# Kernel optimization log

Measured on AMD Instinct MI355X. Metric: run time of the kernel, lower is better.

## Reference

```python
import jax, jax.numpy as jnp
import numpy as np

N_NODES = 50000
N_EDGES = 500000
H = 128
N_LAYERS = 3


def _mlp_params(key, in_dim, h_dim, out_dim):
    k1, k2 = jax.random.split(key)
    s1 = 1.0 / np.sqrt(in_dim)
    s2 = 1.0 / np.sqrt(h_dim)
    return (jax.random.uniform(k1, (in_dim, h_dim), jnp.float32, -s1, s1),
            jnp.zeros((h_dim,), jnp.float32),
            jax.random.uniform(k2, (h_dim, out_dim), jnp.float32, -s2, s2),
            jnp.zeros((out_dim,), jnp.float32))


def setup_inputs() -> dict:
    key = jax.random.key(0)
    ks = jax.random.split(key, 8)
    x = jax.random.normal(ks[0], (N_NODES, H), jnp.float32)
    edge_attr = jax.random.normal(ks[1], (N_EDGES, H), jnp.float32)
    pos = jax.random.normal(ks[2], (N_NODES, 3), jnp.float32)
    src = jax.random.randint(ks[3], (N_EDGES,), 0, N_NODES)
    # avoid self-loops so rel_dist > 0 (original assumes no zero-length edges)
    off = jax.random.randint(ks[4], (N_EDGES,), 1, N_NODES)
    dst = (src + off) % N_NODES
    edge_index = jnp.stack([src, dst]).astype(jnp.int64)
    # per-layer MLP params, stacked over layers
    msg, acc, nod = [], [], []
    for i in range(N_LAYERS):
        kk = jax.random.fold_in(ks[5], i)
        ka, kb, kc = jax.random.split(kk, 3)
        msg.append(_mlp_params(ka, 3 * H, H, H))       # message_mlp
        acc.append(_mlp_params(kb, H, 2 * H, 1))       # accl_mlp
        nod.append(_mlp_params(kc, 2 * H, 2 * H, H))   # node_mlp
    stack = lambda ps: tuple(jnp.stack([p[j] for p in ps]) for j in range(4))
    mW1, mb1, mW2, mb2 = stack(msg)
    aW1, ab1, aW2, ab2 = stack(acc)
    nW1, nb1, nW2, nb2 = stack(nod)
    return dict(x=x, edge_index=edge_index, edge_attr=edge_attr, pos=pos,
                msg_W1=mW1, msg_b1=mb1, msg_W2=mW2, msg_b2=mb2,
                acc_W1=aW1, acc_b1=ab1, acc_W2=aW2, acc_b2=ab2,
                node_W1=nW1, node_b1=nb1, node_W2=nW2, node_b2=nb2)


def _mlp(h, W1, b1, W2, b2):
    return jax.nn.relu(h @ W1 + b1) @ W2 + b2


def reference(x, edge_index, edge_attr, pos,
              msg_W1, msg_b1, msg_W2, msg_b2,
              acc_W1, acc_b1, acc_W2, acc_b2,
              node_W1, node_b1, node_W2, node_b2):
    src, dst = edge_index[0], edge_index[1]
    n = x.shape[0]
    deg = jax.ops.segment_sum(jnp.ones((src.shape[0],), x.dtype), dst, num_segments=n)
    denom = jnp.maximum(deg, 1.0)[:, None]
    for l in range(N_LAYERS):
        # message: cat(x_i=dst, x_j=src, edge_attr) -> MLP
        m_in = jnp.concatenate([x[dst], x[src], edge_attr], axis=-1)  # [E, 3H]
        m = _mlp(m_in, msg_W1[l], msg_b1[l], msg_W2[l], msg_b2[l])    # [E, H]
        # equivariant acceleration update
        w = _mlp(m, acc_W1[l], acc_b1[l], acc_W2[l], acc_b2[l])       # [E, 1]
        rel = pos[src] - pos[dst]                                     # [E, 3]
        dist = jnp.sqrt(jnp.sum(rel * rel, axis=-1, keepdims=True))
        acc_e = w * rel / dist
        pos = pos + jax.ops.segment_sum(acc_e, dst, num_segments=n) / denom
        # node update (beta_x = 1.0 -> x_out = x_update)
        intra = jax.ops.segment_sum(m, dst, num_segments=n) / denom   # [N, H]
        x = _mlp(jnp.concatenate([x, intra], axis=-1),
                 node_W1[l], node_b1[l], node_W2[l], node_b2[l])
    return pos
```

## Files before the change

kernel.cpp:

```cpp
#include <hip/hip_runtime.h>
#include <hip/hip_bf16.h>
#include <math.h>

#define N_NODES 50000
#define N_EDGES 500000
#define H 128
#define NL 3
#define SCAN_B 256
#define NCHUNK ((N_NODES + SCAN_B - 1) / SCAN_B)

typedef short short8v __attribute__((ext_vector_type(8)));
typedef float f32x4 __attribute__((ext_vector_type(4)));
typedef unsigned short ushort8v __attribute__((ext_vector_type(8)));
typedef unsigned short ushort4v __attribute__((ext_vector_type(4)));

__device__ __forceinline__ unsigned short f2b(float f) {
  __hip_bfloat16 h = __float2bfloat16(f);
  return __builtin_bit_cast(unsigned short, h);
}
__device__ __forceinline__ float b2f(unsigned short s) {
  unsigned u = (unsigned)s << 16;
  return __builtin_bit_cast(float, u);
}


__global__ void k_deg_i(const int* __restrict__ dst, int* __restrict__ degC) {
  int e = blockIdx.x * blockDim.x + threadIdx.x;
  if (e < N_EDGES) atomicAdd(&degC[dst[e]], 1);
}

__global__ void k_inv(const int* __restrict__ degC, float* __restrict__ invd) {
  int i = blockIdx.x * blockDim.x + threadIdx.x;
  if (i < N_NODES) invd[i] = 1.0f / fmaxf((float)degC[i], 1.0f);
}

__global__ void k_scan1(const int* __restrict__ degC, int* __restrict__ cursor,
                        int* __restrict__ chunkSum) {
  __shared__ int s[SCAN_B];
  int t = threadIdx.x, i = blockIdx.x * SCAN_B + t;
  int v = (i < N_NODES) ? degC[i] : 0;
  s[t] = v;
  __syncthreads();
  for (int o = 1; o < SCAN_B; o <<= 1) {
    int u = (t >= o) ? s[t - o] : 0;
    __syncthreads();
    s[t] += u;
    __syncthreads();
  }
  if (i < N_NODES) cursor[i] = s[t] - v;
  if (t == SCAN_B - 1) chunkSum[blockIdx.x] = s[t];
}

__global__ void k_scan2(int* __restrict__ chunkSum) {
  __shared__ int s[SCAN_B];
  int t = threadIdx.x;
  int v = (t < NCHUNK) ? chunkSum[t] : 0;
  s[t] = v;
  __syncthreads();
  for (int o = 1; o < SCAN_B; o <<= 1) {
    int u = (t >= o) ? s[t - o] : 0;
    __syncthreads();
    s[t] += u;
    __syncthreads();
  }
  if (t < NCHUNK) chunkSum[t] = s[t] - v;
}

__global__ void k_scan3(int* __restrict__ cursor, const int* __restrict__ chunkSum) {
  int i = blockIdx.x * SCAN_B + threadIdx.x;
  if (i < N_NODES) cursor[i] += chunkSum[blockIdx.x];
}

__global__ void k_scatter_sort(const int* __restrict__ dst, int* __restrict__ cursor,
                               int* __restrict__ sorted) {
  int e = blockIdx.x * blockDim.x + threadIdx.x;
  if (e < N_EDGES) {
    int p = atomicAdd(&cursor[dst[e]], 1);
    sorted[p] = e;
  }
}


__global__ void k_cvt_x(const float* __restrict__ x, unsigned short* __restrict__ xb, int n4) {
  int i = blockIdx.x * blockDim.x + threadIdx.x;
  if (i < n4) {
    float4 v = ((const float4*)x)[i];
    ushort4v o;
    o[0] = f2b(v.x); o[1] = f2b(v.y); o[2] = f2b(v.z); o[3] = f2b(v.w);
    ((ushort4v*)xb)[i] = o;
  }
}

__global__ void k_cvt_wt(const float* __restrict__ src, unsigned short* __restrict__ dst,
                         int K, int N, int total) {
  int i = blockIdx.x * blockDim.x + threadIdx.x;
  if (i < total) {
    int l = i / (K * N);
    int rem = i - l * K * N;
    int k = rem / N;
    int n = rem - k * N;
    dst[((size_t)l * N + n) * K + k] = f2b(src[i]);
  }
}

#define MFMA_STEP(AP, APITCH, AKOFF, ACCN)                                         \
  { _Pragma("unroll")                                                              \
    for (int ks = 0; ks < 2; ++ks) {                                               \
      short8v af_ = *(const short8v*)&AP[(wv * 16 + ln15) * APITCH + (AKOFF) + ks * 32 + quad * 8]; \
      _Pragma("unroll")                                                            \
      for (int nt = 0; nt < 8; ++nt) {                                             \
        short8v bf_ = *(const short8v*)&sB[(nt * 16 + ln15) * 72 + ks * 32 + quad * 8]; \
        ACCN[nt] = __builtin_amdgcn_mfma_f32_16x16x32_bf16(af_, bf_, ACCN[nt], 0, 0, 0); \
      } } }

#define STAGE_B(EXPR)                                                              \
  { _Pragma("unroll")                                                              \
    for (int i_ = 0; i_ < 4; ++i_) {                                               \
      int flat_ = tid + i_ * 256;                                                  \
      int n = flat_ >> 3, seg = flat_ & 7;                                         \
      *(float4*)&sB[n * 72 + seg * 8] = *(const float4*)&(EXPR);                   \
    } }


__launch_bounds__(256, 3)
__global__ void k_edge(const unsigned short* __restrict__ xb,
                       const float* __restrict__ pos,
                       const float* __restrict__ eattr,
                       const int* __restrict__ srcI,
                       const int* __restrict__ dstI,
                       const int* __restrict__ sorted,
                       const unsigned short* __restrict__ mW1t, const float* __restrict__ mb1,
                       const unsigned short* __restrict__ mW2t, const float* __restrict__ mb2,
                       const unsigned short* __restrict__ aW1t, const float* __restrict__ ab1,
                       const float* __restrict__ aW2, const float* __restrict__ ab2,
                       float* __restrict__ intra,
                       float* __restrict__ pdelta,
                       int do_intra)
{
  __shared__ unsigned short sA[64 * 72];
  __shared__ unsigned short sB[128 * 72];
  __shared__ unsigned short sM[64 * 136];
  __shared__ int sEid[64], sSrc[64], sDst[64];
  __shared__ float sW[64];
  __shared__ float sPE[64 * 3];

  const int tid = threadIdx.x;
  const int e0 = blockIdx.x * 64;
  const int nv = min(N_EDGES - e0, 64);
  if (tid < 64) {
    int idx = min(e0 + tid, N_EDGES - 1);
    int eid = sorted[idx];
    sEid[tid] = eid; sSrc[tid] = srcI[eid]; sDst[tid] = dstI[eid];
  }
  __syncthreads();

  const int wv = tid >> 6, lane = tid & 63, quad = lane >> 4, ln15 = lane & 15;

  f32x4 acc[8];
#pragma unroll
  for (int nt = 0; nt < 8; ++nt) acc[nt] = (f32x4){0.f, 0.f, 0.f, 0.f};

  for (int c = 0; c < 6; ++c) {
#pragma unroll
    for (int i_ = 0; i_ < 2; ++i_) {
      int flat_ = tid + i_ * 256;
      int row = flat_ >> 3, seg = flat_ & 7;
      if (c < 4) {
        int node = (c < 2) ? sDst[row] : sSrc[row];
        const unsigned short* sp = xb + (size_t)node * H + (c & 1) * 64 + seg * 8;
        *(float4*)&sA[row * 72 + seg * 8] = *(const float4*)sp;
      } else {
        const float* ep = eattr + (size_t)sEid[row] * H + (c - 4) * 64 + seg * 8;
        float4 p0 = *(const float4*)ep;
        float4 p1 = *(const float4*)(ep + 4);
        ushort8v v;
        v[0] = f2b(p0.x); v[1] = f2b(p0.y); v[2] = f2b(p0.z); v[3] = f2b(p0.w);
        v[4] = f2b(p1.x); v[5] = f2b(p1.y); v[6] = f2b(p1.z); v[7] = f2b(p1.w);
        *(ushort8v*)&sA[row * 72 + seg * 8] = v;
      }
    }
    STAGE_B(mW1t[(size_t)n * 384 + c * 64 + seg * 8])
    __syncthreads();
    MFMA_STEP(sA, 72, 0, acc)
    __syncthreads();
  }

#pragma unroll
  for (int nt = 0; nt < 8; ++nt) {
    int col = nt * 16 + ln15;
    float bb = mb1[col];
#pragma unroll
    for (int r = 0; r < 4; ++r) {
      int row = wv * 16 + quad * 4 + r;
      sM[row * 136 + col] = f2b(fmaxf(acc[nt][r] + bb, 0.f));
      acc[nt][r] = 0.f;
    }
  }
  __syncthreads();

  for (int c = 0; c < 2; ++c) {
    STAGE_B(mW2t[(size_t)n * 128 + c * 64 + seg * 8])
    __syncthreads();
    MFMA_STEP(sM, 136, c * 64, acc)
    __syncthreads();
  }

#pragma unroll
  for (int nt = 0; nt < 8; ++nt) {
    int col = nt * 16 + ln15;
    float bb = mb2[col];
#pragma unroll
    for (int r = 0; r < 4; ++r) {
      int row = wv * 16 + quad * 4 + r;
      sM[row * 136 + col] = f2b(acc[nt][r] + bb);
    }
  }
  __syncthreads();

  float wp0 = 0.f, wp1 = 0.f, wp2 = 0.f, wp3 = 0.f;
  for (int h = 0; h < 2; ++h) {
#pragma unroll
    for (int nt = 0; nt < 8; ++nt) acc[nt] = (f32x4){0.f, 0.f, 0.f, 0.f};
    for (int c = 0; c < 2; ++c) {
      STAGE_B(aW1t[((size_t)h * 128 + n) * 128 + c * 64 + seg * 8])
      __syncthreads();
      MFMA_STEP(sM, 136, c * 64, acc)
      __syncthreads();
    }
#pragma unroll
    for (int nt = 0; nt < 8; ++nt) {
      int col = h * 128 + nt * 16 + ln15;
      float bb = ab1[col], a2 = aW2[col];
      wp0 += fmaxf(acc[nt][0] + bb, 0.f) * a2;
      wp1 += fmaxf(acc[nt][1] + bb, 0.f) * a2;
      wp2 += fmaxf(acc[nt][2] + bb, 0.f) * a2;
      wp3 += fmaxf(acc[nt][3] + bb, 0.f) * a2;
    }
  }
#pragma unroll
  for (int m = 1; m <= 8; m <<= 1) {
    wp0 += __shfl_xor(wp0, m, 64);
    wp1 += __shfl_xor(wp1, m, 64);
    wp2 += __shfl_xor(wp2, m, 64);
    wp3 += __shfl_xor(wp3, m, 64);
  }
  if (ln15 == 0) {
    float b2 = ab2[0];
    sW[wv * 16 + quad * 4 + 0] = wp0 + b2;
    sW[wv * 16 + quad * 4 + 1] = wp1 + b2;
    sW[wv * 16 + quad * 4 + 2] = wp2 + b2;
    sW[wv * 16 + quad * 4 + 3] = wp3 + b2;
  }
  __syncthreads();

  if (tid < nv) {
    int s = sSrc[tid], d = sDst[tid];
    float rx = pos[s * 3 + 0] - pos[d * 3 + 0];
    float ry = pos[s * 3 + 1] - pos[d * 3 + 1];
    float rz = pos[s * 3 + 2] - pos[d * 3 + 2];
    float dist = sqrtf(rx * rx + ry * ry + rz * rz);
    float cf = sW[tid] / dist;
    sPE[tid * 3 + 0] = cf * rx;
    sPE[tid * 3 + 1] = cf * ry;
    sPE[tid * 3 + 2] = cf * rz;
  }
  __syncthreads();

  if (tid < 3) {
    float run = 0.0f;
    int cur = -2;
    for (int e = 0; e < 64; ++e) {
      int d = (e < nv) ? sDst[e] : -1;
      if (d != cur) {
        if (cur >= 0 && run != 0.0f) atomicAdd(&pdelta[cur * 3 + tid], run);
        run = 0.0f;
        cur = d;
      }
      if (d >= 0) run += sPE[e * 3 + tid];
    }
    if (cur >= 0 && run != 0.0f) atomicAdd(&pdelta[cur * 3 + tid], run);
  }

  if (do_intra) {
    int f = tid & 127;
    int hf = tid >> 7;
    int eBeg = hf * 32, eEnd = eBeg + 32;
    float run = 0.0f;
    int cur = -2;
    for (int e = eBeg; e < eEnd; ++e) {
      int d = (e < nv) ? sDst[e] : -1;
      if (d != cur) {
        if (cur >= 0 && run != 0.0f) atomicAdd(&intra[(size_t)cur * H + f], run);
        run = 0.0f;
        cur = d;
      }
      if (d >= 0) run += b2f(sM[e * 136 + f]);
    }
    if (cur >= 0 && run != 0.0f) atomicAdd(&intra[(size_t)cur * H + f], run);
  }
}


__launch_bounds__(256, 3)
__global__ void k_node(const unsigned short* __restrict__ xb,
                       const float* __restrict__ intra,
                       const float* __restrict__ invd,
                       const unsigned short* __restrict__ nW1t, const float* __restrict__ nb1,
                       const unsigned short* __restrict__ nW2t, const float* __restrict__ nb2,
                       const float* __restrict__ pos_in,
                       const float* __restrict__ pdelta,
                       unsigned short* __restrict__ xb_out,
                       float* __restrict__ pos_out,
                       int compute_x)
{
  __shared__ unsigned short sA[64 * 72];
  __shared__ unsigned short sB[128 * 72];
  __shared__ unsigned short sH[64 * 136];
  const int tid = threadIdx.x;
  const int n0 = blockIdx.x * 64;

  if (tid < 192) {
    int n = n0 + tid / 3, cc = tid % 3;
    if (n < N_NODES)
      pos_out[n * 3 + cc] = pos_in[n * 3 + cc] + pdelta[n * 3 + cc] * invd[n];
  }
  if (!compute_x) return;

  const int wv = tid >> 6, lane = tid & 63, quad = lane >> 4, ln15 = lane & 15;

  f32x4 xacc[8];
#pragma unroll
  for (int nt = 0; nt < 8; ++nt) xacc[nt] = (f32x4){0.f, 0.f, 0.f, 0.f};

  f32x4 acc[8];
  for (int h = 0; h < 2; ++h) {
#pragma unroll
    for (int nt = 0; nt < 8; ++nt) acc[nt] = (f32x4){0.f, 0.f, 0.f, 0.f};
    for (int c = 0; c < 4; ++c) {
#pragma unroll
      for (int i_ = 0; i_ < 2; ++i_) {
        int flat_ = tid + i_ * 256;
        int row = flat_ >> 3, seg = flat_ & 7;
        int n = min(n0 + row, N_NODES - 1);
        if (c < 2) {
          *(float4*)&sA[row * 72 + seg * 8] =
              *(const float4*)&xb[(size_t)n * H + c * 64 + seg * 8];
        } else {
          const float* ip = intra + (size_t)n * H + (c - 2) * 64 + seg * 8;
          float iv = invd[n];
          float4 p0 = *(const float4*)ip;
          float4 p1 = *(const float4*)(ip + 4);
          ushort8v v;
          v[0] = f2b(p0.x * iv); v[1] = f2b(p0.y * iv);
          v[2] = f2b(p0.z * iv); v[3] = f2b(p0.w * iv);
          v[4] = f2b(p1.x * iv); v[5] = f2b(p1.y * iv);
          v[6] = f2b(p1.z * iv); v[7] = f2b(p1.w * iv);
          *(ushort8v*)&sA[row * 72 + seg * 8] = v;
        }
      }
      STAGE_B(nW1t[((size_t)h * 128 + n) * 256 + c * 64 + seg * 8])
      __syncthreads();
      MFMA_STEP(sA, 72, 0, acc)
      __syncthreads();
    }
#pragma unroll
    for (int nt = 0; nt < 8; ++nt) {
      int col = nt * 16 + ln15;
      float bb = nb1[h * 128 + col];
#pragma unroll
      for (int r = 0; r < 4; ++r) {
        int row = wv * 16 + quad * 4 + r;
        sH[row * 136 + col] = f2b(fmaxf(acc[nt][r] + bb, 0.f));
      }
    }
    __syncthreads();
    for (int c2 = 0; c2 < 2; ++c2) {
      STAGE_B(nW2t[(size_t)n * 256 + h * 128 + c2 * 64 + seg * 8])
      __syncthreads();
      MFMA_STEP(sH, 136, c2 * 64, xacc)
      __syncthreads();
    }
  }
#pragma unroll
  for (int nt = 0; nt < 8; ++nt) {
    int col = nt * 16 + ln15;
    float bb = nb2[col];
#pragma unroll
    for (int r = 0; r < 4; ++r) {
      int row = n0 + wv * 16 + quad * 4 + r;
      if (row < N_NODES)
        xb_out[(size_t)row * H + col] = f2b(xacc[nt][r] + bb);
    }
  }
}

extern "C" void kernel_launch(void* const* d_in, const int* in_sizes, int n_in,
                              void* d_out, int out_size, void* d_ws, size_t ws_size,
                              hipStream_t stream) {
  const float* x0    = (const float*)d_in[0];
  const int*   eidx  = (const int*)d_in[1];
  const float* eattr = (const float*)d_in[2];
  const float* pos0  = (const float*)d_in[3];
  const float* mW1 = (const float*)d_in[4];
  const float* mb1 = (const float*)d_in[5];
  const float* mW2 = (const float*)d_in[6];
  const float* mb2 = (const float*)d_in[7];
  const float* aW1 = (const float*)d_in[8];
  const float* ab1 = (const float*)d_in[9];
  const float* aW2 = (const float*)d_in[10];
  const float* ab2 = (const float*)d_in[11];
  const float* nW1 = (const float*)d_in[12];
  const float* nb1 = (const float*)d_in[13];
  const float* nW2 = (const float*)d_in[14];
  const float* nb2 = (const float*)d_in[15];
  const int* srcI = eidx;
  const int* dstI = eidx + N_EDGES;

  char* wsb = (char*)d_ws;
  int*   degC    = (int*)wsb;                     wsb += (size_t)N_NODES * 4;
  int*   cursor  = (int*)wsb;                     wsb += (size_t)N_NODES * 4;
  int*   chunkS  = (int*)wsb;                     wsb += 256 * 4;
  int*   sorted  = (int*)wsb;                     wsb += (size_t)N_EDGES * 4;
  float* invd    = (float*)wsb;                   wsb += (size_t)N_NODES * 4;
  float* pdelta  = (float*)wsb;                   wsb += (size_t)3 * N_NODES * 4;
  float* pos_a   = (float*)wsb;                   wsb += (size_t)3 * N_NODES * 4;
  float* pos_b   = (float*)wsb;                   wsb += (size_t)3 * N_NODES * 4;
  float* intra   = (float*)wsb;                   wsb += (size_t)N_NODES * H * 4;
  unsigned short* xb0  = (unsigned short*)wsb;    wsb += (size_t)N_NODES * H * 2;
  unsigned short* xb_a = (unsigned short*)wsb;    wsb += (size_t)N_NODES * H * 2;
  unsigned short* xb_b = (unsigned short*)wsb;    wsb += (size_t)N_NODES * H * 2;
  unsigned short* mW1t = (unsigned short*)wsb;    wsb += (size_t)NL * 128 * 384 * 2;
  unsigned short* mW2t = (unsigned short*)wsb;    wsb += (size_t)NL * 128 * 128 * 2;
  unsigned short* aW1t = (unsigned short*)wsb;    wsb += (size_t)NL * 256 * 128 * 2;
  unsigned short* nW1t = (unsigned short*)wsb;    wsb += (size_t)NL * 256 * 256 * 2;
  unsigned short* nW2t = (unsigned short*)wsb;    wsb += (size_t)NL * 128 * 256 * 2;

  hipMemsetAsync(degC, 0, N_NODES * sizeof(int), stream);
  k_deg_i<<<(N_EDGES + 255) / 256, 256, 0, stream>>>(dstI, degC);
  k_inv<<<(N_NODES + 255) / 256, 256, 0, stream>>>(degC, invd);
  k_scan1<<<NCHUNK, SCAN_B, 0, stream>>>(degC, cursor, chunkS);
  k_scan2<<<1, SCAN_B, 0, stream>>>(chunkS);
  k_scan3<<<NCHUNK, SCAN_B, 0, stream>>>(cursor, chunkS);
  k_scatter_sort<<<(N_EDGES + 255) / 256, 256, 0, stream>>>(dstI, cursor, sorted);

  {
    int n4 = N_NODES * H / 4;
    k_cvt_x<<<(n4 + 255) / 256, 256, 0, stream>>>(x0, xb0, n4);
    int t1 = NL * 384 * 128;
    k_cvt_wt<<<(t1 + 255) / 256, 256, 0, stream>>>(mW1, mW1t, 384, 128, t1);
    int t2 = NL * 128 * 128;
    k_cvt_wt<<<(t2 + 255) / 256, 256, 0, stream>>>(mW2, mW2t, 128, 128, t2);
    int t3 = NL * 128 * 256;
    k_cvt_wt<<<(t3 + 255) / 256, 256, 0, stream>>>(aW1, aW1t, 128, 256, t3);
    int t4 = NL * 256 * 256;
    k_cvt_wt<<<(t4 + 255) / 256, 256, 0, stream>>>(nW1, nW1t, 256, 256, t4);
    int t5 = NL * 256 * 128;
    k_cvt_wt<<<(t5 + 255) / 256, 256, 0, stream>>>(nW2, nW2t, 256, 128, t5);
  }

  const unsigned short* xc = xb0;
  const float* pc = pos0;
  float* pos_out_final = (float*)d_out;

  for (int l = 0; l < NL; ++l) {
    int last = (l == NL - 1);
    hipMemsetAsync(pdelta, 0, 3 * N_NODES * sizeof(float), stream);
    if (!last)
      hipMemsetAsync(intra, 0, (size_t)N_NODES * H * sizeof(float), stream);

    k_edge<<<(N_EDGES + 63) / 64, 256, 0, stream>>>(
        xc, pc, eattr, srcI, dstI, sorted,
        mW1t + (size_t)l * 128 * 384, mb1 + (size_t)l * 128,
        mW2t + (size_t)l * 128 * 128, mb2 + (size_t)l * 128,
        aW1t + (size_t)l * 256 * 128, ab1 + (size_t)l * 256,
        aW2 + (size_t)l * 256, ab2 + l,
        intra, pdelta, last ? 0 : 1);

    float* pn = last ? pos_out_final : (l == 0 ? pos_a : pos_b);
    unsigned short* xn = (l == 0) ? xb_a : xb_b;
    k_node<<<(N_NODES + 63) / 64, 256, 0, stream>>>(
        xc, intra, invd,
        nW1t + (size_t)l * 256 * 256, nb1 + (size_t)l * 256,
        nW2t + (size_t)l * 128 * 256, nb2 + (size_t)l * 128,
        pc, pdelta, xn, pn, last ? 0 : 1);

    xc = xn;
    pc = pn;
  }
}
```

Before: 1.386 ms.

## Precompute per-node projections of the message MLP's first layer

The first message-MLP layer is split by linearity. The x_dst and x_src parts are computed once per node in a new k_xab kernel and stored as bf16. Each edge then gathers and adds the two projected rows and only runs the edge_attr part of the GEMM (K=128 instead of 384). This cuts per-edge MFMA work and replaces gathers of raw features with gathers of precomputed projections. The costs are an extra kernel, a 256-wide bf16 buffer, and extra bf16 rounding of the partial sums. It also loads edge_attr A fragments directly into registers and raises the launch-bounds occupancy hint from 3 to 4.

```diff
diff --git a/kernel.cpp b/kernel.cpp
--- a/kernel.cpp
+++ b/kernel.cpp
@@ -122,8 +122,57 @@
     } }
 
 
-__launch_bounds__(256, 3)
-__global__ void k_edge(const unsigned short* __restrict__ xb,
+__launch_bounds__(256, 4)
+__global__ void k_xab(const unsigned short* __restrict__ xb,
+                      const unsigned short* __restrict__ mW1t,
+                      unsigned short* __restrict__ xab)
+{
+  __shared__ unsigned short sB[128 * 72];
+  const int tid = threadIdx.x;
+  const int n0 = blockIdx.x * 64;
+  const int wv = tid >> 6, lane = tid & 63, quad = lane >> 4, ln15 = lane & 15;
+  const int arow = min(n0 + wv * 16 + ln15, N_NODES - 1);
+
+  short8v afr[2][2];
+#pragma unroll
+  for (int c = 0; c < 2; ++c)
+#pragma unroll
+    for (int ks = 0; ks < 2; ++ks)
+      afr[c][ks] = *(const short8v*)&xb[(size_t)arow * H + c * 64 + ks * 32 + quad * 8];
+
+  for (int h = 0; h < 2; ++h) {
+    f32x4 acc[8];
+#pragma unroll
+    for (int nt = 0; nt < 8; ++nt) acc[nt] = (f32x4){0.f, 0.f, 0.f, 0.f};
+    for (int c = 0; c < 2; ++c) {
+      STAGE_B(mW1t[(size_t)n * 384 + h * 128 + c * 64 + seg * 8])
+      __syncthreads();
+#pragma unroll
+      for (int ks = 0; ks < 2; ++ks) {
+#pragma unroll
+        for (int nt = 0; nt < 8; ++nt) {
+          short8v bf = *(const short8v*)&sB[(nt * 16 + ln15) * 72 + ks * 32 + quad * 8];
+          acc[nt] = __builtin_amdgcn_mfma_f32_16x16x32_bf16(afr[c][ks], bf, acc[nt], 0, 0, 0);
+        }
+      }
+      __syncthreads();
+    }
+#pragma unroll
+    for (int nt = 0; nt < 8; ++nt) {
+      int col = nt * 16 + ln15;
+#pragma unroll
+      for (int r = 0; r < 4; ++r) {
+        int row = n0 + wv * 16 + quad * 4 + r;
+        if (row < N_NODES)
+          xab[(size_t)row * 256 + h * 128 + col] = f2b(acc[nt][r]);
+      }
+    }
+  }
+}
+
+
+__launch_bounds__(256, 4)
+__global__ void k_edge(const unsigned short* __restrict__ xab,
                        const float* __restrict__ pos,
                        const float* __restrict__ eattr,
                        const int* __restrict__ srcI,
@@ -137,7 +186,6 @@
                        float* __restrict__ pdelta,
                        int do_intra)
 {
-  __shared__ unsigned short sA[64 * 72];
   __shared__ unsigned short sB[128 * 72];
   __shared__ unsigned short sM[64 * 136];
   __shared__ int sEid[64], sSrc[64], sDst[64];
@@ -156,32 +204,49 @@
 
   const int wv = tid >> 6, lane = tid & 63, quad = lane >> 4, ln15 = lane & 15;
 
+#pragma unroll
+  for (int i_ = 0; i_ < 4; ++i_) {
+    int flat = tid + i_ * 256;
+    int row = flat >> 4, sg = flat & 15;
+    ushort8v a = *(const ushort8v*)&xab[(size_t)sDst[row] * 256 + sg * 8];
+    ushort8v b = *(const ushort8v*)&xab[(size_t)sSrc[row] * 256 + 128 + sg * 8];
+    ushort8v o;
+#pragma unroll
+    for (int j = 0; j < 8; ++j) o[j] = f2b(b2f(a[j]) + b2f(b[j]));
+    *(ushort8v*)&sM[row * 136 + sg * 8] = o;
+  }
+
   f32x4 acc[8];
 #pragma unroll
   for (int nt = 0; nt < 8; ++nt) acc[nt] = (f32x4){0.f, 0.f, 0.f, 0.f};
 
-  for (int c = 0; c < 6; ++c) {
-#pragma unroll
-    for (int i_ = 0; i_ < 2; ++i_) {
-      int flat_ = tid + i_ * 256;
-      int row = flat_ >> 3, seg = flat_ & 7;
-      if (c < 4) {
-        int node = (c < 2) ? sDst[row] : sSrc[row];
-        const unsigned short* sp = xb + (size_t)node * H + (c & 1) * 64 + seg * 8;
-        *(float4*)&sA[row * 72 + seg * 8] = *(const float4*)sp;
-      } else {
-        const float* ep = eattr + (size_t)sEid[row] * H + (c - 4) * 64 + seg * 8;
-        float4 p0 = *(const float4*)ep;
-        float4 p1 = *(const float4*)(ep + 4);
-        ushort8v v;
-        v[0] = f2b(p0.x); v[1] = f2b(p0.y); v[2] = f2b(p0.z); v[3] = f2b(p0.w);
-        v[4] = f2b(p1.x); v[5] = f2b(p1.y); v[6] = f2b(p1.z); v[7] = f2b(p1.w);
-        *(ushort8v*)&sA[row * 72 + seg * 8] = v;
-      }
-    }
-    STAGE_B(mW1t[(size_t)n * 384 + c * 64 + seg * 8])
-    __syncthreads();
-    MFMA_STEP(sA, 72, 0, acc)
+  const float* aep = eattr + (size_t)sEid[wv * 16 + ln15] * H;
+  for (int c = 0; c < 2; ++c) {
+    float4 q0 = *(const float4*)(aep + c * 64 + quad * 8);
+    float4 q1 = *(const float4*)(aep + c * 64 + quad * 8 + 4);
+    float4 q2 = *(const float4*)(aep + c * 64 + 32 + quad * 8);
+    float4 q3 = *(const float4*)(aep + c * 64 + 32 + quad * 8 + 4);
+    STAGE_B(mW1t[(size_t)n * 384 + 256 + c * 64 + seg * 8])
+    __syncthreads();
+    short8v af0, af1;
+    af0[0] = (short)f2b(q0.x); af0[1] = (short)f2b(q0.y);
+    af0[2] = (short)f2b(q0.z); af0[3] = (short)f2b(q0.w);
+    af0[4] = (short)f2b(q1.x); af0[5] = (short)f2b(q1.y);
+    af0[6] = (short)f2b(q1.z); af0[7] = (short)f2b(q1.w);
+    af1[0] = (short)f2b(q2.x); af1[1] = (short)f2b(q2.y);
+    af1[2] = (short)f2b(q2.z); af1[3] = (short)f2b(q2.w);
+    af1[4] = (short)f2b(q3.x); af1[5] = (short)f2b(q3.y);
+    af1[6] = (short)f2b(q3.z); af1[7] = (short)f2b(q3.w);
+#pragma unroll
+    for (int nt = 0; nt < 8; ++nt) {
+      short8v bf = *(const short8v*)&sB[(nt * 16 + ln15) * 72 + quad * 8];
+      acc[nt] = __builtin_amdgcn_mfma_f32_16x16x32_bf16(af0, bf, acc[nt], 0, 0, 0);
+    }
+#pragma unroll
+    for (int nt = 0; nt < 8; ++nt) {
+      short8v bf = *(const short8v*)&sB[(nt * 16 + ln15) * 72 + 32 + quad * 8];
+      acc[nt] = __builtin_amdgcn_mfma_f32_16x16x32_bf16(af1, bf, acc[nt], 0, 0, 0);
+    }
     __syncthreads();
   }
 
@@ -192,7 +257,8 @@
 #pragma unroll
     for (int r = 0; r < 4; ++r) {
       int row = wv * 16 + quad * 4 + r;
-      sM[row * 136 + col] = f2b(fmaxf(acc[nt][r] + bb, 0.f));
+      float xv = b2f(sM[row * 136 + col]);
+      sM[row * 136 + col] = f2b(fmaxf(acc[nt][r] + xv + bb, 0.f));
       acc[nt][r] = 0.f;
     }
   }
@@ -429,6 +495,7 @@
   unsigned short* xb0  = (unsigned short*)wsb;    wsb += (size_t)N_NODES * H * 2;
   unsigned short* xb_a = (unsigned short*)wsb;    wsb += (size_t)N_NODES * H * 2;
   unsigned short* xb_b = (unsigned short*)wsb;    wsb += (size_t)N_NODES * H * 2;
+  unsigned short* xabW = (unsigned short*)wsb;    wsb += (size_t)N_NODES * 256 * 2;
   unsigned short* mW1t = (unsigned short*)wsb;    wsb += (size_t)NL * 128 * 384 * 2;
   unsigned short* mW2t = (unsigned short*)wsb;    wsb += (size_t)NL * 128 * 128 * 2;
   unsigned short* aW1t = (unsigned short*)wsb;    wsb += (size_t)NL * 256 * 128 * 2;
@@ -468,8 +535,11 @@
     if (!last)
       hipMemsetAsync(intra, 0, (size_t)N_NODES * H * sizeof(float), stream);
 
+    k_xab<<<(N_NODES + 63) / 64, 256, 0, stream>>>(
+        xc, mW1t + (size_t)l * 128 * 384, xabW);
+
     k_edge<<<(N_EDGES + 63) / 64, 256, 0, stream>>>(
-        xc, pc, eattr, srcI, dstI, sorted,
+        xabW, pc, eattr, srcI, dstI, sorted,
         mW1t + (size_t)l * 128 * 384, mb1 + (size_t)l * 128,
         mW2t + (size_t)l * 128 * 128, mb2 + (size_t)l * 128,
         aW1t + (size_t)l * 256 * 128, ab1 + (size_t)l * 256,
```

Measured after the change: 1.466 ms. 1.06x slower.
